# Kernel tuning notes

Measured on AMD Instinct MI355X. Metric: run time of the kernel, lower is better.

The kernel has to match this reference:

```python
import jax, jax.numpy as jnp
import numpy as np


def _layernorm(x, g, b, eps=1e-5):
    m = jnp.mean(x, axis=-1, keepdims=True)
    v = jnp.var(x, axis=-1, keepdims=True)
    return (x - m) / jnp.sqrt(v + eps) * g + b


def setup_inputs() -> dict:
    key = jax.random.key(0)
    ks = jax.random.split(key, 18)
    B, H, W, E = 16, 64, 64, 512
    F = 2048          # ff_dim = 4 * embed_dim
    d = E // 8        # reduced Q/K channel dim from in_dim // 8
    L = 512           # max_len for relative position tables
    s = 0.02
    rn = lambda k, shape: (jax.random.normal(k, shape, jnp.float32) * s)
    return {
        "x": jax.random.normal(ks[0], (B, H, W, E), jnp.float32),
        "Wq": rn(ks[1], (E, d)), "bq": jnp.zeros((d,), jnp.float32),
        "Wk": rn(ks[2], (E, d)), "bk": jnp.zeros((d,), jnp.float32),
        "Wv": rn(ks[3], (E, E)), "bv": jnp.zeros((E,), jnp.float32),
        "rel_h": jax.random.normal(ks[4], (L, d), jnp.float32),
        "rel_w": jax.random.normal(ks[5], (L, d), jnp.float32),
        "ln1_g": jnp.ones((E,), jnp.float32), "ln1_b": jnp.zeros((E,), jnp.float32),
        "W1": rn(ks[6], (E, F)), "b1": jnp.zeros((F,), jnp.float32),
        "W2": rn(ks[7], (F, E)), "b2": jnp.zeros((E,), jnp.float32),
        "ln2_g": jnp.ones((E,), jnp.float32), "ln2_b": jnp.zeros((E,), jnp.float32),
    }


def reference(x, Wq, bq, Wk, bk, Wv, bv, rel_h, rel_w,
              ln1_g, ln1_b, W1, b1, W2, b2, ln2_g, ln2_b):
    B, H, W_, E = x.shape
    # 1x1 convs == per-pixel linear projections (channels-last)
    q = x @ Wq + bq + rel_h[:H][:, None, :]   # (B,H,W,d) + height pos emb on queries
    k = x @ Wk + bk + rel_w[:W_]              # (B,H,W,d) + width pos emb on keys
    v = x @ Wv + bv                           # (B,H,W,E)
    # axial attention along the width axis (no sqrt(d) scaling, as in source)
    attn = jax.nn.softmax(jnp.einsum('bhid,bhjd->bhij', q, k), axis=-1)  # (B,H,W,W)
    attn_out = jnp.einsum('bhij,bhje->bhie', attn, v)                    # (B,H,W,E)
    # residual + LN (dropout is identity in eval mode)
    h1 = _layernorm(x + attn_out, ln1_g, ln1_b)
    # FFN: Linear -> GELU(exact, torch default) -> Linear
    ffn = jax.nn.gelu(h1 @ W1 + b1, approximate=False) @ W2 + b2
    return _layernorm(h1 + ffn, ln2_g, ln2_b)
```

## Files before the change

kernel.cpp:

```cpp
#include <hip/hip_runtime.h>
#include <stdint.h>

typedef unsigned short u16;
typedef __attribute__((ext_vector_type(4))) float f32x4;
typedef __attribute__((ext_vector_type(8))) short bf16x8;
typedef __attribute__((ext_vector_type(8))) unsigned short u16x8;

__device__ __forceinline__ u16 f2b(float f) {
    union { float f; unsigned u; } x; x.f = f;
    unsigned r = x.u + 0x7fffu + ((x.u >> 16) & 1u);
    return (u16)(r >> 16);
}
__device__ __forceinline__ float b2f(u16 b) {
    union { unsigned u; float f; } x; x.u = ((unsigned)b) << 16;
    return x.f;
}

__global__ __launch_bounds__(256) void k_cast(const float* __restrict__ s, u16* __restrict__ d) {
    size_t i = (size_t)blockIdx.x * 256 + threadIdx.x;
    const f32x4* sp = (const f32x4*)(s + i * 8);
    f32x4 a = sp[0], b = sp[1];
    u16x8 o;
    o[0] = f2b(a[0]); o[1] = f2b(a[1]); o[2] = f2b(a[2]); o[3] = f2b(a[3]);
    o[4] = f2b(b[0]); o[5] = f2b(b[1]); o[6] = f2b(b[2]); o[7] = f2b(b[3]);
    *(u16x8*)(d + i * 8) = o;
}

__global__ __launch_bounds__(256) void k_transpose(const float* __restrict__ src, u16* __restrict__ dst,
                                                   int M, int dstOff, int dstStride) {
    __shared__ float t[32][33];
    int bx = blockIdx.x * 32;
    int by = blockIdx.y * 32;
    int tx = threadIdx.x & 31, ty = threadIdx.x >> 5;
#pragma unroll
    for (int r = 0; r < 32; r += 8)
        t[ty + r][tx] = src[(size_t)(bx + ty + r) * M + by + tx];
    __syncthreads();
#pragma unroll
    for (int r = 0; r < 32; r += 8)
        dst[(size_t)(dstOff + by + ty + r) * dstStride + bx + tx] = f2b(t[tx][ty + r]);
}

__device__ __forceinline__ void tile_map(int bid, int nR, int nC, int G, int& tr, int& tc) {
    int nwg = nR * nC;
    int q = nwg >> 3, r8 = nwg & 7;
    int xcd = bid & 7, idx = bid >> 3;
    int swz = (xcd < r8 ? xcd * (q + 1) : r8 * (q + 1) + (xcd - r8) * q) + idx;
    int per = G * nC;
    int s = swz / per, w = swz % per;
    int rbase = s * G;
    int g = nR - rbase; if (g > G) g = G;
    tr = rbase + w % g;
    tc = w / g;
}

template<int EPI>
__global__ __launch_bounds__(256) void k_gemm(
    const u16* __restrict__ A, const u16* __restrict__ BT, u16* __restrict__ C, int K,
    int M, int nR, int nC, int G,
    const float* __restrict__ bias0, const float* __restrict__ bias1, const float* __restrict__ bias2,
    const float* __restrict__ relh, const float* __restrict__ relw)
{
    __shared__ __align__(16) u16 As[128 * 64];
    __shared__ __align__(16) u16 Bs[128 * 64];
    const int lane = threadIdx.x & 63;
    const int wid  = threadIdx.x >> 6;
    int tr, tc;
    tile_map((int)blockIdx.x, nR, nC, G, tr, tc);
    const int rowBase = tr * 128;
    const int colBase = tc * 128;
    const int wr = (wid >> 1) * 64;
    const int wc = (wid & 1) * 64;

    const int srow   = lane >> 3;
    const int schunk = (lane & 7) ^ srow;

    f32x4 acc[4][4] = {};

    const u16* gA = A  + (size_t)(rowBase + srow) * K + schunk * 8;
    const u16* gB = BT + (size_t)(colBase + srow) * K + schunk * 8;

    for (int k0 = 0; k0 < K; k0 += 64) {
#pragma unroll
        for (int i = 0; i < 4; ++i) {
            int ii = i * 4 + wid;
            __builtin_amdgcn_global_load_lds(
                (const __attribute__((address_space(1))) void*)(gA + (size_t)ii * 8 * K + k0),
                (__attribute__((address_space(3))) void*)&As[ii * 512], 16, 0, 0);
            __builtin_amdgcn_global_load_lds(
                (const __attribute__((address_space(1))) void*)(gB + (size_t)ii * 8 * K + k0),
                (__attribute__((address_space(3))) void*)&Bs[ii * 512], 16, 0, 0);
        }
        __syncthreads();
#pragma unroll
        for (int kk = 0; kk < 2; ++kk) {
            const int cc = (kk * 4 + (lane >> 4)) ^ (lane & 7);
            bf16x8 af[4], bfr[4];
#pragma unroll
            for (int m = 0; m < 4; ++m) {
                int row = wr + m * 16 + (lane & 15);
                af[m] = *(const bf16x8*)&As[row * 64 + cc * 8];
            }
#pragma unroll
            for (int n = 0; n < 4; ++n) {
                int row = wc + n * 16 + (lane & 15);
                bfr[n] = *(const bf16x8*)&Bs[row * 64 + cc * 8];
            }
#pragma unroll
            for (int m = 0; m < 4; ++m)
#pragma unroll
                for (int n = 0; n < 4; ++n)
                    acc[m][n] = __builtin_amdgcn_mfma_f32_16x16x32_bf16(af[m], bfr[n], acc[m][n], 0, 0, 0);
        }
        __syncthreads();
    }

#pragma unroll
    for (int m = 0; m < 4; ++m) {
        int grow0 = rowBase + wr + m * 16 + ((lane >> 4) << 2);
#pragma unroll
        for (int n = 0; n < 4; ++n) {
            int gcol = colBase + wc + n * 16 + (lane & 15);
            float badd;
            if (EPI == 0) {
                badd = (gcol < 64) ? bias0[gcol] : (gcol < 128 ? bias1[gcol - 64] : bias2[gcol - 128]);
            } else {
                badd = bias0[gcol];
            }
#pragma unroll
            for (int p = 0; p < 4; ++p) {
                int r = grow0 + p;
                float v = acc[m][n][p] + badd;
                if (EPI == 0) {
                    if (gcol < 64)        v += relh[(((r >> 6) & 63) << 6) + gcol];
                    else if (gcol < 128)  v += relw[((r & 63) << 6) + (gcol - 64)];
                } else if (EPI == 1) {
                    v = 0.5f * v * (1.0f + erff(v * 0.70710678118654752f));
                }
                C[(size_t)r * M + gcol] = f2b(v);
            }
        }
    }
}

__global__ __launch_bounds__(256) void k_attn(const u16* __restrict__ qkv, u16* __restrict__ ao) {
    __shared__ __align__(16) u16 vsT[512 * 64];
    __shared__ __align__(16) u16 ps[64 * 72];
    const int lane = threadIdx.x & 63;
    const int wid  = threadIdx.x >> 6;
    const int t    = threadIdx.x;
    const size_t base = (size_t)blockIdx.x * 64;

    for (int it = 0; it < 16; ++it) {
        int idx = t + it * 256;
        int j   = idx >> 6;
        int c0  = (idx & 63) * 8;
        bf16x8 vv = *(const bf16x8*)(qkv + (base + j) * 640 + 128 + c0);
#pragma unroll
        for (int e = 0; e < 8; ++e) {
            int c = c0 + e;
            vsT[c * 64 + (j ^ ((c & 7) << 3))] = (u16)vv[e];
        }
    }

    const int r0 = wid * 16;
    const int g  = lane >> 4;
    bf16x8 qa[2];
#pragma unroll
    for (int kk = 0; kk < 2; ++kk)
        qa[kk] = *(const bf16x8*)(qkv + (base + r0 + (lane & 15)) * 640 + kk * 32 + (g << 3));
    f32x4 s[4] = {};
#pragma unroll
    for (int n = 0; n < 4; ++n)
#pragma unroll
        for (int kk = 0; kk < 2; ++kk) {
            bf16x8 kb = *(const bf16x8*)(qkv + (base + n * 16 + (lane & 15)) * 640 + 64 + kk * 32 + (g << 3));
            s[n] = __builtin_amdgcn_mfma_f32_16x16x32_bf16(qa[kk], kb, s[n], 0, 0, 0);
        }

    float mx[4], sm[4], inv[4];
    float pe[4][4];
#pragma unroll
    for (int p = 0; p < 4; ++p)
        mx[p] = fmaxf(fmaxf(s[0][p], s[1][p]), fmaxf(s[2][p], s[3][p]));
#pragma unroll
    for (int d = 1; d < 16; d <<= 1)
#pragma unroll
        for (int p = 0; p < 4; ++p) mx[p] = fmaxf(mx[p], __shfl_xor(mx[p], d));
#pragma unroll
    for (int p = 0; p < 4; ++p) sm[p] = 0.f;
#pragma unroll
    for (int n = 0; n < 4; ++n)
#pragma unroll
        for (int p = 0; p < 4; ++p) { pe[n][p] = __expf(s[n][p] - mx[p]); sm[p] += pe[n][p]; }
#pragma unroll
    for (int d = 1; d < 16; d <<= 1)
#pragma unroll
        for (int p = 0; p < 4; ++p) sm[p] += __shfl_xor(sm[p], d);
#pragma unroll
    for (int p = 0; p < 4; ++p) inv[p] = 1.f / sm[p];
#pragma unroll
    for (int n = 0; n < 4; ++n)
#pragma unroll
        for (int p = 0; p < 4; ++p)
            ps[(r0 + (g << 2) + p) * 72 + n * 16 + (lane & 15)] = f2b(pe[n][p] * inv[p]);

    __syncthreads();

    bf16x8 pa[2];
#pragma unroll
    for (int kk = 0; kk < 2; ++kk)
        pa[kk] = *(const bf16x8*)&ps[(r0 + (lane & 15)) * 72 + kk * 32 + (g << 3)];
    for (int n = 0; n < 32; ++n) {
        f32x4 o = {};
#pragma unroll
        for (int kk = 0; kk < 2; ++kk) {
            int c  = n * 16 + (lane & 15);
            int cl = kk * 4 + g;
            bf16x8 vb = *(const bf16x8*)&vsT[c * 64 + ((cl ^ (c & 7)) << 3)];
            o = __builtin_amdgcn_mfma_f32_16x16x32_bf16(pa[kk], vb, o, 0, 0, 0);
        }
        int col = n * 16 + (lane & 15);
#pragma unroll
        for (int p = 0; p < 4; ++p)
            ao[(base + r0 + (g << 2) + p) * 512 + col] = f2b(o[p]);
    }
}

__global__ __launch_bounds__(256) void k_ln1(const float* __restrict__ x, const u16* __restrict__ ao,
                                             const float* __restrict__ gw, const float* __restrict__ gb,
                                             u16* __restrict__ h1) {
    const int lane = threadIdx.x & 63;
    const size_t row = (size_t)blockIdx.x * 4 + (threadIdx.x >> 6);
    const size_t off = row * 512 + lane * 8;
    f32x4 x0 = *(const f32x4*)(x + off), x1 = *(const f32x4*)(x + off + 4);
    u16x8 a = *(const u16x8*)(ao + off);
    float v[8];
    v[0]=x0[0]+b2f(a[0]); v[1]=x0[1]+b2f(a[1]); v[2]=x0[2]+b2f(a[2]); v[3]=x0[3]+b2f(a[3]);
    v[4]=x1[0]+b2f(a[4]); v[5]=x1[1]+b2f(a[5]); v[6]=x1[2]+b2f(a[6]); v[7]=x1[3]+b2f(a[7]);
    float s = 0.f, q = 0.f;
#pragma unroll
    for (int i = 0; i < 8; ++i) { s += v[i]; q += v[i] * v[i]; }
#pragma unroll
    for (int d = 1; d < 64; d <<= 1) { s += __shfl_xor(s, d); q += __shfl_xor(q, d); }
    float mean = s * (1.f / 512.f);
    float var  = q * (1.f / 512.f) - mean * mean;
    float rstd = rsqrtf(var + 1e-5f);
    u16x8 o;
#pragma unroll
    for (int i = 0; i < 8; ++i)
        o[i] = f2b((v[i] - mean) * rstd * gw[lane * 8 + i] + gb[lane * 8 + i]);
    *(u16x8*)(h1 + off) = o;
}

__global__ __launch_bounds__(256) void k_ln2(const u16* __restrict__ h1, const u16* __restrict__ ff,
                                             const float* __restrict__ gw, const float* __restrict__ gb,
                                             float* __restrict__ out) {
    const int lane = threadIdx.x & 63;
    const size_t row = (size_t)blockIdx.x * 4 + (threadIdx.x >> 6);
    const size_t off = row * 512 + lane * 8;
    u16x8 a = *(const u16x8*)(h1 + off);
    u16x8 c = *(const u16x8*)(ff + off);
    float v[8];
#pragma unroll
    for (int i = 0; i < 8; ++i) v[i] = b2f(a[i]) + b2f(c[i]);
    float s = 0.f, q = 0.f;
#pragma unroll
    for (int i = 0; i < 8; ++i) { s += v[i]; q += v[i] * v[i]; }
#pragma unroll
    for (int d = 1; d < 64; d <<= 1) { s += __shfl_xor(s, d); q += __shfl_xor(q, d); }
    float mean = s * (1.f / 512.f);
    float var  = q * (1.f / 512.f) - mean * mean;
    float rstd = rsqrtf(var + 1e-5f);
    f32x4 o0, o1;
#pragma unroll
    for (int i = 0; i < 4; ++i) o0[i] = (v[i] - mean) * rstd * gw[lane * 8 + i] + gb[lane * 8 + i];
#pragma unroll
    for (int i = 0; i < 4; ++i) o1[i] = (v[4 + i] - mean) * rstd * gw[lane * 8 + 4 + i] + gb[lane * 8 + 4 + i];
    *(f32x4*)(out + off) = o0;
    *(f32x4*)(out + off + 4) = o1;
}

extern "C" void kernel_launch(void* const* d_in, const int* in_sizes, int n_in,
                              void* d_out, int out_size, void* d_ws, size_t ws_size,
                              hipStream_t stream) {
    const float* x    = (const float*)d_in[0];
    const float* Wq   = (const float*)d_in[1];
    const float* bq   = (const float*)d_in[2];
    const float* Wk   = (const float*)d_in[3];
    const float* bk   = (const float*)d_in[4];
    const float* Wv   = (const float*)d_in[5];
    const float* bv   = (const float*)d_in[6];
    const float* relh = (const float*)d_in[7];
    const float* relw = (const float*)d_in[8];
    const float* g1   = (const float*)d_in[9];
    const float* bb1  = (const float*)d_in[10];
    const float* W1   = (const float*)d_in[11];
    const float* b1   = (const float*)d_in[12];
    const float* W2   = (const float*)d_in[13];
    const float* b2   = (const float*)d_in[14];
    const float* g2   = (const float*)d_in[15];
    const float* bb2  = (const float*)d_in[16];
    float* out = (float*)d_out;

    char* ws = (char*)d_ws;
    u16* u     = (u16*)(ws + 0);
    u16* xb    = (u16*)(ws + 0);
    u16* qkv   = (u16*)(ws + 67108864ull);
    u16* ao    = (u16*)(ws + 150994944ull);
    u16* h1    = (u16*)(ws + 268435456ull);
    u16* ff2   = (u16*)(ws + 335544320ull);
    u16* wqkvT = (u16*)(ws + 402653184ull);
    u16* w1T   = (u16*)(ws + 403308544ull);
    u16* w2T   = (u16*)(ws + 405405696ull);

    k_transpose<<<dim3(16, 2),  256, 0, stream>>>(Wq, wqkvT, 64,   0,   512);
    k_transpose<<<dim3(16, 2),  256, 0, stream>>>(Wk, wqkvT, 64,   64,  512);
    k_transpose<<<dim3(16, 16), 256, 0, stream>>>(Wv, wqkvT, 512,  128, 512);
    k_transpose<<<dim3(16, 64), 256, 0, stream>>>(W1, w1T,   2048, 0,   512);
    k_transpose<<<dim3(64, 16), 256, 0, stream>>>(W2, w2T,   512,  0,   2048);

    k_cast<<<16384, 256, 0, stream>>>(x, xb);

    k_gemm<0><<<512 * 5,  256, 0, stream>>>(xb, wqkvT, qkv, 512,  640,  512, 5,  8, bq, bk, bv, relh, relw);
    k_attn<<<1024, 256, 0, stream>>>(qkv, ao);
    k_ln1<<<16384, 256, 0, stream>>>(x, ao, g1, bb1, h1);
    k_gemm<1><<<512 * 16, 256, 0, stream>>>(h1, w1T, u,   512,  2048, 512, 16, 8, b1, nullptr, nullptr, nullptr, nullptr);
    k_gemm<2><<<512 * 4,  256, 0, stream>>>(u,  w2T, ff2, 2048, 512,  512, 4,  2, b2, nullptr, nullptr, nullptr, nullptr);
    k_ln2<<<16384, 256, 0, stream>>>(h1, ff2, g2, bb2, out);
}
```

Baseline: 722.6 us.

## Add 256x256 multi-stage pipelined GEMM kernel for FFN matmuls

Introduces a new 512-thread GEMM kernel with 256x256 output tiles, a 4-deep LDS ring buffer fed by async global-to-LDS loads, explicit vmcnt/lgkmcnt waits, split barriers and MFMA priority hints. It is used for both FFN GEMMs, replacing the 128x128 single-buffered kernel. The intent is to raise arithmetic intensity per tile and overlap global loads with MFMA work. In exchange it uses far more registers and 128KB of LDS per block, and the hand-placed waitcnt counts must stay in step with the issued loads. The erf-GELU epilogue is removed from the old kernel because that path is no longer called.

```diff
diff --git a/kernel.cpp b/kernel.cpp
--- a/kernel.cpp
+++ b/kernel.cpp
@@ -15,6 +15,12 @@
     union { unsigned u; float f; } x; x.u = ((unsigned)b) << 16;
     return x.f;
 }
+
+#define ASM_VMCNT(n) do { asm volatile("s_waitcnt vmcnt(" #n ")" ::: "memory"); __builtin_amdgcn_sched_barrier(0); } while (0)
+#define ASM_LGKM0()  do { asm volatile("s_waitcnt lgkmcnt(0)" ::: "memory"); __builtin_amdgcn_sched_barrier(0); } while (0)
+#define GLOAD16(g, l) __builtin_amdgcn_global_load_lds( \
+    (const __attribute__((address_space(1))) void*)(g), \
+    (__attribute__((address_space(3))) void*)(l), 16, 0, 0)
 
 __global__ __launch_bounds__(256) void k_cast(const float* __restrict__ s, u16* __restrict__ d) {
     size_t i = (size_t)blockIdx.x * 256 + threadIdx.x;
@@ -52,6 +58,128 @@
     int g = nR - rbase; if (g > G) g = G;
     tr = rbase + w % g;
     tc = w / g;
+}
+
+template<int EPI>
+__global__ __launch_bounds__(512, 2) void k_gemm256(
+    const u16* __restrict__ A, const u16* __restrict__ BT, u16* __restrict__ C, int K,
+    int M, int nR, int nC, int G, const float* __restrict__ bias)
+{
+    __shared__ __align__(16) u16 sm[4 * 16384];
+    const int tid  = threadIdx.x;
+    const int lane = tid & 63;
+    const int wid  = tid >> 6;
+    const int wm   = wid >> 2;
+    const int wn   = wid & 3;
+    int tr, tc;
+    tile_map((int)blockIdx.x, nR, nC, G, tr, tc);
+    const int rowBase = tr * 256;
+    const int colBase = tc * 256;
+    const int NT = K >> 5;
+
+    const int srow = tid >> 2;
+    const int scol = ((tid & 3) ^ ((tid >> 3) & 3)) * 8;
+    const u16* gA0 = A  + (size_t)(rowBase + srow) * K + scol;
+    const u16* gB0 = BT + (size_t)(colBase + srow) * K + scol;
+    const size_t instStep = (size_t)128 * K;
+    u16* ldsW = sm + wid * 512;
+
+    const int rbA   = wm * 128 + (lane & 15);
+    const int rbB   = wn * 64  + (lane & 15);
+    const int offA0 = rbA * 32 + (((lane >> 4) ^ ((rbA >> 1) & 3)) * 8);
+    const int offB0 = rbB * 32 + (((lane >> 4) ^ ((rbB >> 1) & 3)) * 8);
+
+    f32x4 acc[8][4] = {};
+
+#pragma unroll
+    for (int tt = 0; tt < 3; ++tt) {
+        const u16* ga = gA0 + (size_t)tt * 32;
+        const u16* gb = gB0 + (size_t)tt * 32;
+        u16* la = ldsW + tt * 16384;
+        u16* lb = la + 8192;
+        GLOAD16(ga, la);
+        GLOAD16(ga + instStep, la + 4096);
+        GLOAD16(gb, lb);
+        GLOAD16(gb + instStep, lb + 4096);
+    }
+    ASM_VMCNT(8);
+    __builtin_amdgcn_s_barrier();
+
+    for (int t = 0; t < NT; ++t) {
+        const u16* Ab = &sm[(t & 3) * 16384];
+        const u16* Bb = Ab + 8192;
+        const int tt = t + 3;
+        const bool doStage = (tt < NT);
+        const u16* ga = gA0 + (size_t)tt * 32;
+        const u16* gb = gB0 + (size_t)tt * 32;
+        u16* la = ldsW + (tt & 3) * 16384;
+        u16* lb = la + 8192;
+
+        bf16x8 bf0 = *(const bf16x8*)&Bb[offB0];
+        bf16x8 bf1 = *(const bf16x8*)&Bb[offB0 + 512];
+        bf16x8 bf2 = *(const bf16x8*)&Bb[offB0 + 1024];
+        bf16x8 bf3 = *(const bf16x8*)&Bb[offB0 + 1536];
+        bf16x8 a0 = *(const bf16x8*)&Ab[offA0];
+        bf16x8 a1 = *(const bf16x8*)&Ab[offA0 + 512];
+        bf16x8 a2 = *(const bf16x8*)&Ab[offA0 + 1024];
+        bf16x8 a3 = *(const bf16x8*)&Ab[offA0 + 1536];
+        if (doStage) { GLOAD16(ga, la); GLOAD16(ga + instStep, la + 4096); }
+        __builtin_amdgcn_s_barrier();
+        ASM_LGKM0();
+        __builtin_amdgcn_s_setprio(1);
+#pragma unroll
+        for (int n = 0; n < 4; ++n) {
+            const bf16x8 bb = (n == 0) ? bf0 : (n == 1) ? bf1 : (n == 2) ? bf2 : bf3;
+            acc[0][n] = __builtin_amdgcn_mfma_f32_16x16x32_bf16(a0, bb, acc[0][n], 0, 0, 0);
+            acc[1][n] = __builtin_amdgcn_mfma_f32_16x16x32_bf16(a1, bb, acc[1][n], 0, 0, 0);
+            acc[2][n] = __builtin_amdgcn_mfma_f32_16x16x32_bf16(a2, bb, acc[2][n], 0, 0, 0);
+            acc[3][n] = __builtin_amdgcn_mfma_f32_16x16x32_bf16(a3, bb, acc[3][n], 0, 0, 0);
+        }
+        __builtin_amdgcn_s_setprio(0);
+        __builtin_amdgcn_s_barrier();
+
+        bf16x8 a4 = *(const bf16x8*)&Ab[offA0 + 2048];
+        bf16x8 a5 = *(const bf16x8*)&Ab[offA0 + 2560];
+        bf16x8 a6 = *(const bf16x8*)&Ab[offA0 + 3072];
+        bf16x8 a7 = *(const bf16x8*)&Ab[offA0 + 3584];
+        if (doStage) { GLOAD16(gb, lb); GLOAD16(gb + instStep, lb + 4096); }
+        __builtin_amdgcn_s_barrier();
+        ASM_LGKM0();
+        __builtin_amdgcn_s_setprio(1);
+#pragma unroll
+        for (int n = 0; n < 4; ++n) {
+            const bf16x8 bb = (n == 0) ? bf0 : (n == 1) ? bf1 : (n == 2) ? bf2 : bf3;
+            acc[4][n] = __builtin_amdgcn_mfma_f32_16x16x32_bf16(a4, bb, acc[4][n], 0, 0, 0);
+            acc[5][n] = __builtin_amdgcn_mfma_f32_16x16x32_bf16(a5, bb, acc[5][n], 0, 0, 0);
+            acc[6][n] = __builtin_amdgcn_mfma_f32_16x16x32_bf16(a6, bb, acc[6][n], 0, 0, 0);
+            acc[7][n] = __builtin_amdgcn_mfma_f32_16x16x32_bf16(a7, bb, acc[7][n], 0, 0, 0);
+        }
+        __builtin_amdgcn_s_setprio(0);
+
+        if (t < NT - 1) {
+            const int rem = NT - t - 2;
+            if (rem >= 2)      ASM_VMCNT(8);
+            else if (rem == 1) ASM_VMCNT(4);
+            else               ASM_VMCNT(0);
+            __builtin_amdgcn_s_barrier();
+        }
+    }
+
+#pragma unroll
+    for (int f = 0; f < 8; ++f) {
+        const int grow0 = rowBase + wm * 128 + f * 16 + ((lane >> 4) << 2);
+#pragma unroll
+        for (int n = 0; n < 4; ++n) {
+            const int gcol = colBase + wn * 64 + n * 16 + (lane & 15);
+            const float badd = bias[gcol];
+#pragma unroll
+            for (int p = 0; p < 4; ++p) {
+                float v = acc[f][n][p] + badd;
+                if (EPI == 1) v = 0.5f * v * (1.0f + erff(v * 0.70710678118654752f));
+                C[(size_t)(grow0 + p) * M + gcol] = f2b(v);
+            }
+        }
+    }
 }
 
 template<int EPI>
@@ -84,12 +212,8 @@
 #pragma unroll
         for (int i = 0; i < 4; ++i) {
             int ii = i * 4 + wid;
-            __builtin_amdgcn_global_load_lds(
-                (const __attribute__((address_space(1))) void*)(gA + (size_t)ii * 8 * K + k0),
-                (__attribute__((address_space(3))) void*)&As[ii * 512], 16, 0, 0);
-            __builtin_amdgcn_global_load_lds(
-                (const __attribute__((address_space(1))) void*)(gB + (size_t)ii * 8 * K + k0),
-                (__attribute__((address_space(3))) void*)&Bs[ii * 512], 16, 0, 0);
+            GLOAD16(gA + (size_t)ii * 8 * K + k0, &As[ii * 512]);
+            GLOAD16(gB + (size_t)ii * 8 * K + k0, &Bs[ii * 512]);
         }
         __syncthreads();
 #pragma unroll
@@ -134,8 +258,6 @@
                 if (EPI == 0) {
                     if (gcol < 64)        v += relh[(((r >> 6) & 63) << 6) + gcol];
                     else if (gcol < 128)  v += relw[((r & 63) << 6) + (gcol - 64)];
-                } else if (EPI == 1) {
-                    v = 0.5f * v * (1.0f + erff(v * 0.70710678118654752f));
                 }
                 C[(size_t)r * M + gcol] = f2b(v);
             }
@@ -178,7 +300,7 @@
             s[n] = __builtin_amdgcn_mfma_f32_16x16x32_bf16(qa[kk], kb, s[n], 0, 0, 0);
         }
 
-    float mx[4], sm[4], inv[4];
+    float mx[4], sm2[4], inv[4];
     float pe[4][4];
 #pragma unroll
     for (int p = 0; p < 4; ++p)
@@ -188,17 +310,17 @@
 #pragma unroll
         for (int p = 0; p < 4; ++p) mx[p] = fmaxf(mx[p], __shfl_xor(mx[p], d));
 #pragma unroll
-    for (int p = 0; p < 4; ++p) sm[p] = 0.f;
+    for (int p = 0; p < 4; ++p) sm2[p] = 0.f;
 #pragma unroll
     for (int n = 0; n < 4; ++n)
 #pragma unroll
-        for (int p = 0; p < 4; ++p) { pe[n][p] = __expf(s[n][p] - mx[p]); sm[p] += pe[n][p]; }
+        for (int p = 0; p < 4; ++p) { pe[n][p] = __expf(s[n][p] - mx[p]); sm2[p] += pe[n][p]; }
 #pragma unroll
     for (int d = 1; d < 16; d <<= 1)
 #pragma unroll
-        for (int p = 0; p < 4; ++p) sm[p] += __shfl_xor(sm[p], d);
-#pragma unroll
-    for (int p = 0; p < 4; ++p) inv[p] = 1.f / sm[p];
+        for (int p = 0; p < 4; ++p) sm2[p] += __shfl_xor(sm2[p], d);
+#pragma unroll
+    for (int p = 0; p < 4; ++p) inv[p] = 1.f / sm2[p];
 #pragma unroll
     for (int n = 0; n < 4; ++n)
 #pragma unroll
@@ -325,7 +447,7 @@
     k_gemm<0><<<512 * 5,  256, 0, stream>>>(xb, wqkvT, qkv, 512,  640,  512, 5,  8, bq, bk, bv, relh, relw);
     k_attn<<<1024, 256, 0, stream>>>(qkv, ao);
     k_ln1<<<16384, 256, 0, stream>>>(x, ao, g1, bb1, h1);
-    k_gemm<1><<<512 * 16, 256, 0, stream>>>(h1, w1T, u,   512,  2048, 512, 16, 8, b1, nullptr, nullptr, nullptr, nullptr);
-    k_gemm<2><<<512 * 4,  256, 0, stream>>>(u,  w2T, ff2, 2048, 512,  512, 4,  2, b2, nullptr, nullptr, nullptr, nullptr);
+    k_gemm256<1><<<256 * 8, 512, 0, stream>>>(h1, w1T, u,   512,  2048, 256, 8, 8, b1);
+    k_gemm256<2><<<256 * 2, 512, 0, stream>>>(u,  w2T, ff2, 2048, 512,  256, 2, 2, b2);
     k_ln2<<<16384, 256, 0, stream>>>(h1, ff2, g2, bb2, out);
 }
```

After: 738.9 us. +2.3%, slower.
